# Kernel tuning notes

Measured on AMD Instinct MI355X. Metric: run time of the kernel, lower is better.

## Reference

```python
import jax, jax.numpy as jnp
import numpy as np

B, S, D = 32, 8192, 128
SPARSITY = 0.5
CLUSTER = 4
HID = 256
MEM = 128
NCLS = 10
MASK_KEY = jax.random.key(1234)


def setup_inputs() -> dict:
    key = jax.random.key(0)
    ks = jax.random.split(key, 8)
    cin = CLUSTER * D  # 512
    return {
        "x": jax.random.normal(ks[0], (B, S, D), dtype=jnp.float32),
        "memory": jax.random.normal(ks[1], (B, MEM), dtype=jnp.float32),
        "W_fc": jax.random.normal(ks[2], (HID, cin), dtype=jnp.float32) / np.sqrt(cin),
        "b_fc": jax.random.normal(ks[3], (HID,), dtype=jnp.float32) * 0.01,
        "W_mem": jax.random.normal(ks[4], (MEM, HID), dtype=jnp.float32) / np.sqrt(HID),
        "b_mem": jax.random.normal(ks[5], (MEM,), dtype=jnp.float32) * 0.01,
        "W_out": jax.random.normal(ks[6], (NCLS, MEM), dtype=jnp.float32) / np.sqrt(MEM),
        "b_out": jax.random.normal(ks[7], (NCLS,), dtype=jnp.float32) * 0.01,
    }


def reference(x, memory, W_fc, b_fc, W_mem, b_mem, W_out, b_out):
    # --- SparseInformationExtraction: top-k tokens by L2 norm ---
    k = int(SPARSITY * S)  # 4096
    token_norms = jnp.linalg.norm(x, axis=-1)          # (B, S)
    _, topk_idx = jax.lax.top_k(token_norms, k)        # (B, k), sorted desc like torch.topk
    sparse_x = jnp.take_along_axis(x, topk_idx[:, :, None], axis=1)  # (B, k, D)

    # --- HierarchicalClustering: group CLUSTER tokens ---
    num_clusters = k // CLUSTER                        # 1024
    clustered = sparse_x.reshape(B, num_clusters, CLUSTER * D)  # (B, 1024, 512)

    # --- DynamicMaskingActivation: linear + bernoulli mask + relu ---
    h = jnp.einsum('bnc,hc->bnh', clustered, W_fc) + b_fc       # (B, 1024, HID)
    mask = jax.random.bernoulli(MASK_KEY, p=SPARSITY, shape=h.shape).astype(h.dtype)
    h = jax.nn.relu(h * mask)

    # --- SparseMemory: mean-pool + linear + residual relu ---
    x_compressed = jnp.mean(h, axis=1)                           # (B, HID)
    updated_memory = jax.nn.relu(x_compressed @ W_mem.T + b_mem + memory)  # (B, MEM)

    # --- output head ---
    output = updated_memory @ W_out.T + b_out                    # (B, NCLS)
    return (output, updated_memory)
```

## Files before the change

### kernel.cpp

```cpp
#include <hip/hip_runtime.h>
#include <stdint.h>

#define NB 32
#define NS 8192
#define ND 128
#define KTOP 4096
#define NCLUST 1024
#define CIN 512
#define HIDN 256
#define NMEM 128
#define NCLS 10
#define HALFCNT 4194304u

typedef unsigned long long ull;
typedef __attribute__((ext_vector_type(8))) short bf16x8;
typedef __attribute__((ext_vector_type(4))) float f32x4;

__device__ __forceinline__ unsigned int rotl32(unsigned int v, int r) {
  return (v << r) | (v >> (32 - r));
}

__device__ __forceinline__ void threefry_block(unsigned int& x0, unsigned int& x1) {
  const unsigned int k0 = 0u;
  const unsigned int k1 = 1234u;
  const unsigned int k2 = 0x1BD11BDAu ^ 0u ^ 1234u;
  x0 += k0; x1 += k1;
#define TF_R(r) { x0 += x1; x1 = rotl32(x1, (r)); x1 ^= x0; }
  TF_R(13) TF_R(15) TF_R(26) TF_R(6)   x0 += k1; x1 += k2 + 1u;
  TF_R(17) TF_R(29) TF_R(16) TF_R(24)  x0 += k2; x1 += k0 + 2u;
  TF_R(13) TF_R(15) TF_R(26) TF_R(6)   x0 += k0; x1 += k1 + 3u;
  TF_R(17) TF_R(29) TF_R(16) TF_R(24)  x0 += k1; x1 += k2 + 4u;
  TF_R(13) TF_R(15) TF_R(26) TF_R(6)   x0 += k2; x1 += k0 + 5u;
#undef TF_R
}

__device__ __forceinline__ unsigned int f2bf(float f) {
  unsigned int u = __float_as_uint(f);
  return (u + 0x7fffu + ((u >> 16) & 1u)) >> 16;
}
__device__ __forceinline__ unsigned int pack2bf(float lo, float hi) {
  return f2bf(lo) | (f2bf(hi) << 16);
}

__device__ __forceinline__ void gload_lds16(const void* g, void* l) {
  __builtin_amdgcn_global_load_lds(
      (const __attribute__((address_space(1))) unsigned int*)g,
      (__attribute__((address_space(3))) unsigned int*)l, 16, 0, 0);
}

__device__ __forceinline__ ull shfl_xor_u64(ull x, int m) {
  unsigned int lo = (unsigned int)x, hi = (unsigned int)(x >> 32);
  lo = (unsigned int)__shfl_xor((int)lo, m);
  hi = (unsigned int)__shfl_xor((int)hi, m);
  return ((ull)hi << 32) | lo;
}

#define NORM_BLOCKS 32768
#define WPREP_BLOCKS 64
#define MASK_BLOCKS 16384
__global__ __launch_bounds__(256) void norms_kernel(
    const float* __restrict__ x, ull* __restrict__ keys,
    float* __restrict__ xc, const float* __restrict__ Wfc,
    unsigned short* __restrict__ Wbf, ull* __restrict__ maskw) {
  const int blk = blockIdx.x;
  if (blk >= NORM_BLOCKS + WPREP_BLOCKS) {
    const int blkm = blk - (NORM_BLOCKS + WPREP_BLOCKS);
    const int wv = threadIdx.x >> 6, lane = threadIdx.x & 63;
    const unsigned int W = (unsigned int)(blkm * 4 + wv);
    unsigned int a = W * 64u + (unsigned int)lane;
    unsigned int b2 = a + HALFCNT;
    threefry_block(a, b2);
    const ull m0 = __ballot((a & 0x80000000u) == 0u);
    const ull m1 = __ballot((b2 & 0x80000000u) == 0u);
    if (lane == 0) {
      maskw[W] = m0;
      maskw[W + 65536u] = m1;
    }
    return;
  }
  if (blk >= NORM_BLOCKS) {
    const int t = (blk - NORM_BLOCKS) * 256 + threadIdx.x;
    const float4* s = (const float4*)(Wfc + (size_t)t * 8);
    const float4 a = s[0], b = s[1];
    uint4 o;
    o.x = pack2bf(a.x, a.y); o.y = pack2bf(a.z, a.w);
    o.z = pack2bf(b.x, b.y); o.w = pack2bf(b.z, b.w);
    *(uint4*)(Wbf + (size_t)t * 8) = o;
    return;
  }
  const int t = blk * 256 + threadIdx.x;
  if (t < NB * HIDN) xc[t] = 0.0f;
  const int token = t >> 5;
  const int l = t & 31;
  const float4 v = ((const float4*)(x + (size_t)token * ND))[l];
  float ss = v.x * v.x + v.y * v.y + v.z * v.z + v.w * v.w;
#pragma unroll
  for (int off = 16; off >= 1; off >>= 1) ss += __shfl_xor(ss, off);
  if (l == 0) {
    const float nrm = sqrtf(ss);
    const unsigned int ub = ~__float_as_uint(nrm);
    keys[token] = ((ull)ub << 32) | (unsigned int)(token & (NS - 1));
  }
}

#define CMPEX(J, K, HF)                                                 \
  {                                                                     \
    _Pragma("unroll") for (int r = 0; r < 8; ++r) {                     \
      if ((r & (J)) == 0) {                                             \
        const int i0 = (tid << 3) + r;                                  \
        const bool up2 = (((i0 & (K)) == 0) != (HF));                   \
        const ull lo = v[r], hi = v[r | (J)];                           \
        const ull mn = lo < hi ? lo : hi;                               \
        const ull mx = lo < hi ? hi : lo;                               \
        v[r] = up2 ? mn : mx;                                           \
        v[r | (J)] = up2 ? mx : mn;                                     \
      }                                                                 \
    }                                                                   \
  }

__global__ __launch_bounds__(512) void sortA_kernel(ull* __restrict__ keys) {
  __shared__ ull slds[8 * 512];
  const int b = blockIdx.x >> 1;
  const int half = blockIdx.x & 1;
  const bool hf = (half != 0);
  const int tid = threadIdx.x;
  ull v[8];
  ull* base = keys + (size_t)b * NS + half * 4096;
#pragma unroll
  for (int r = 0; r < 8; ++r) v[r] = base[tid * 8 + r];

  for (int k = 2; k <= 4096; k <<= 1) {
    for (int j = k >> 1; j >= 512; j >>= 1) {
      __syncthreads();
#pragma unroll
      for (int r = 0; r < 8; ++r) slds[r * 512 + tid] = v[r];
      __syncthreads();
      const int ptid = tid ^ (j >> 3);
      const bool up2 = ((((tid << 3) & k) == 0) != hf);
      const bool lower = (((tid << 3) & j) == 0);
      const bool keepmin = (up2 == lower);
#pragma unroll
      for (int r = 0; r < 8; ++r) {
        const ull p = slds[r * 512 + ptid];
        const ull mn = v[r] < p ? v[r] : p;
        const ull mx = v[r] < p ? p : v[r];
        v[r] = keepmin ? mn : mx;
      }
    }
    {
      const int jstart = (k >> 1) < 256 ? (k >> 1) : 256;
      for (int j = jstart; j >= 8; j >>= 1) {
        const int lanemask = j >> 3;
        const bool up2 = ((((tid << 3) & k) == 0) != hf);
        const bool lower = (((tid << 3) & j) == 0);
        const bool keepmin = (up2 == lower);
#pragma unroll
        for (int r = 0; r < 8; ++r) {
          const ull p = shfl_xor_u64(v[r], lanemask);
          const ull mn = v[r] < p ? v[r] : p;
          const ull mx = v[r] < p ? p : v[r];
          v[r] = keepmin ? mn : mx;
        }
      }
    }
    if (k >= 8)      { CMPEX(4, k, hf) CMPEX(2, k, hf) CMPEX(1, k, hf) }
    else if (k == 4) { CMPEX(2, k, hf) CMPEX(1, k, hf) }
    else             { CMPEX(1, k, hf) }
  }

#pragma unroll
  for (int r = 0; r < 8; ++r) base[tid * 8 + r] = v[r];
}

__global__ __launch_bounds__(512) void sortB_kernel(
    const ull* __restrict__ keys, unsigned int* __restrict__ topk) {
  __shared__ ull slds[8 * 512];
  const int b = blockIdx.x;
  const int tid = threadIdx.x;
  ull v[8];
  const ull* base = keys + (size_t)b * NS;
#pragma unroll
  for (int r = 0; r < 8; ++r) v[r] = base[tid * 8 + r];
#pragma unroll
  for (int r = 0; r < 8; ++r) {
    const ull u = base[4096 + tid * 8 + r];
    v[r] = v[r] < u ? v[r] : u;
  }
  for (int j = 2048; j >= 512; j >>= 1) {
    __syncthreads();
#pragma unroll
    for (int r = 0; r < 8; ++r) slds[r * 512 + tid] = v[r];
    __syncthreads();
    const int ptid = tid ^ (j >> 3);
    const bool keepmin = (((tid << 3) & j) == 0);
#pragma unroll
    for (int r = 0; r < 8; ++r) {
      const ull p = slds[r * 512 + ptid];
      const ull mn = v[r] < p ? v[r] : p;
      const ull mx = v[r] < p ? p : v[r];
      v[r] = keepmin ? mn : mx;
    }
  }
  for (int j = 256; j >= 8; j >>= 1) {
    const int lanemask = j >> 3;
    const bool keepmin = (((tid << 3) & j) == 0);
#pragma unroll
    for (int r = 0; r < 8; ++r) {
      const ull p = shfl_xor_u64(v[r], lanemask);
      const ull mn = v[r] < p ? v[r] : p;
      const ull mx = v[r] < p ? p : v[r];
      v[r] = keepmin ? mn : mx;
    }
  }
  CMPEX(4, 8192, false) CMPEX(2, 8192, false) CMPEX(1, 8192, false)
#pragma unroll
  for (int r = 0; r < 8; ++r)
    topk[b * KTOP + tid * 8 + r] = (unsigned int)v[r];
}

__global__ __launch_bounds__(256, 4) void gemm_kernel(
    const float* __restrict__ x, const unsigned short* __restrict__ Wbf,
    const float* __restrict__ bfc, const unsigned int* __restrict__ topk,
    const ull* __restrict__ maskw, float* __restrict__ xc) {
  __shared__ __align__(16) unsigned short Al[32 * 64];
  __shared__ __align__(16) unsigned short Bl[256 * 64];
  __shared__ int tokL[128];

  const int bid = blockIdx.x;
  const int bb = bid >> 5;
  const int m0c = (bid & 31) * 32;
  const int t = threadIdx.x;
  const int w = t >> 6, l = t & 63;
  const int lrow = l & 15, lk = l >> 4;

  if (t < 128)
    tokL[t] = (int)topk[bb * KTOP + (m0c + (t >> 2)) * 4 + (t & 3)];
  __syncthreads();

  const int arow = t >> 3, kq = t & 7;
  float4 ar[16];
  {
    const float* xb = x + (size_t)bb * NS * ND;
#pragma unroll
    for (int kt = 0; kt < 8; ++kt) {
      const int cs = kt * 8 + kq;
      const int token = tokL[arow * 4 + (cs >> 4)];
      const float* asrc = xb + (size_t)token * ND + (cs & 15) * 8;
      ar[kt * 2]     = ((const float4*)asrc)[0];
      ar[kt * 2 + 1] = ((const float4*)asrc)[1];
    }
  }

  f32x4 acc[2][4];
#pragma unroll
  for (int m = 0; m < 2; ++m)
#pragma unroll
    for (int n = 0; n < 4; ++n) acc[m][n] = (f32x4)0.f;

  const int brow_in8 = l >> 3;
  const int bkb_src = ((l & 7) * 16) ^ (brow_in8 << 4);

  for (int kt = 0; kt < 8; ++kt) {
    {
      const float4 a0 = ar[kt * 2], a1 = ar[kt * 2 + 1];
      uint4 p0;
      p0.x = pack2bf(a0.x, a0.y); p0.y = pack2bf(a0.z, a0.w);
      p0.z = pack2bf(a1.x, a1.y); p0.w = pack2bf(a1.z, a1.w);
      const int swz = (arow & 7) << 4;
      *(uint4*)((char*)Al + arow * 128 + ((kq * 16) ^ swz)) = p0;
    }
    {
#pragma unroll
      for (int q = 0; q < 8; ++q) {
        const int grp = w * 8 + q;
        const int row = grp * 8 + brow_in8;
        const char* g = (const char*)Wbf + (size_t)row * 1024 + kt * 128 +
                        bkb_src;
        gload_lds16(g, (char*)Bl + grp * 1024);
      }
    }
    __syncthreads();

    const int swz = (lrow & 7) << 4;
#pragma unroll
    for (int kk = 0; kk < 2; ++kk) {
      const int koff = (kk * 64 + lk * 16) ^ swz;
      bf16x8 af[2], bfr[4];
#pragma unroll
      for (int m = 0; m < 2; ++m)
        af[m] = *(const bf16x8*)((const char*)Al +
                                 (m * 16 + lrow) * 128 + koff);
#pragma unroll
      for (int n = 0; n < 4; ++n)
        bfr[n] = *(const bf16x8*)((const char*)Bl +
                                  (w * 64 + n * 16 + lrow) * 128 + koff);
#pragma unroll
      for (int m = 0; m < 2; ++m)
#pragma unroll
        for (int n = 0; n < 4; ++n)
          acc[m][n] = __builtin_amdgcn_mfma_f32_16x16x32_bf16(
              af[m], bfr[n], acc[m][n], 0, 0, 0);
    }
    __syncthreads();
  }

  float bias_n[4];
#pragma unroll
  for (int n = 0; n < 4; ++n) bias_n[n] = bfc[w * 64 + n * 16 + lrow];

  ull mw[2][4];
#pragma unroll
  for (int m = 0; m < 2; ++m)
#pragma unroll
    for (int reg = 0; reg < 4; ++reg) {
      const int row = m0c + m * 16 + lk * 4 + reg;
      mw[m][reg] = maskw[(size_t)(bb * NCLUST + row) * 4 + w];
    }

  float csum[4] = {0.f, 0.f, 0.f, 0.f};
#pragma unroll
  for (int n = 0; n < 4; ++n) {
    const int bit = n * 16 + lrow;
#pragma unroll
    for (int m = 0; m < 2; ++m) {
#pragma unroll
      for (int reg = 0; reg < 4; ++reg) {
        const bool keep = ((mw[m][reg] >> bit) & 1ull) != 0ull;
        float vv = acc[m][n][reg] + bias_n[n];
        vv = keep ? fmaxf(vv, 0.0f) : 0.0f;
        csum[n] += vv;
      }
    }
  }
#pragma unroll
  for (int n = 0; n < 4; ++n) {
    csum[n] += __shfl_xor(csum[n], 16);
    csum[n] += __shfl_xor(csum[n], 32);
  }
  if (l < 16) {
#pragma unroll
    for (int n = 0; n < 4; ++n)
      atomicAdd(&xc[bb * HIDN + w * 64 + n * 16 + l], csum[n]);
  }
}

__global__ __launch_bounds__(128) void tail_kernel(
    const float* __restrict__ xc, const float* __restrict__ memory,
    const float* __restrict__ Wmem, const float* __restrict__ bmem,
    const float* __restrict__ Wout, const float* __restrict__ bout,
    float* __restrict__ out) {
  __shared__ __align__(16) float xl[HIDN];
  __shared__ float ul[NMEM];
  const int b = blockIdx.x, t = threadIdx.x;
  xl[t]       = xc[b * HIDN + t] * (1.0f / NCLUST);
  xl[t + 128] = xc[b * HIDN + t + 128] * (1.0f / NCLUST);
  __syncthreads();
  float a = 0.0f;
  const float4* wr2 = (const float4*)(Wmem + (size_t)t * HIDN);
#pragma unroll 4
  for (int q = 0; q < HIDN / 4; ++q) {
    const float4 wv = wr2[q];
    const float4 xv = *(const float4*)&xl[q * 4];
    a = fmaf(wv.x, xv.x, a); a = fmaf(wv.y, xv.y, a);
    a = fmaf(wv.z, xv.z, a); a = fmaf(wv.w, xv.w, a);
  }
  a += bmem[t] + memory[b * NMEM + t];
  a = fmaxf(a, 0.0f);
  ul[t] = a;
  out[NB * NCLS + b * NMEM + t] = a;
  __syncthreads();
  if (t < NCLS) {
    float o = 0.0f;
#pragma unroll 4
    for (int m = 0; m < NMEM; ++m) o = fmaf(ul[m], Wout[t * NMEM + m], o);
    out[b * NCLS + t] = o + bout[t];
  }
}

extern "C" void kernel_launch(void* const* d_in, const int* in_sizes, int n_in,
                              void* d_out, int out_size, void* d_ws, size_t ws_size,
                              hipStream_t stream) {
  (void)in_sizes; (void)n_in; (void)out_size; (void)ws_size;
  const float* x    = (const float*)d_in[0];
  const float* mem  = (const float*)d_in[1];
  const float* Wfc  = (const float*)d_in[2];
  const float* bfc  = (const float*)d_in[3];
  const float* Wmem = (const float*)d_in[4];
  const float* bmem = (const float*)d_in[5];
  const float* Wout = (const float*)d_in[6];
  const float* bout = (const float*)d_in[7];
  float* out = (float*)d_out;

  char* ws = (char*)d_ws;
  size_t off = 0;
  ull* keys = (ull*)(ws + off);          off += (size_t)NB * NS * 8;
  unsigned int* topk = (unsigned int*)(ws + off); off += (size_t)NB * KTOP * 4;
  float* xc = (float*)(ws + off);        off += (size_t)NB * HIDN * 4;
  unsigned short* Wbf = (unsigned short*)(ws + off); off += (size_t)HIDN * CIN * 2;
  ull* maskw = (ull*)(ws + off);

  norms_kernel<<<dim3(NORM_BLOCKS + WPREP_BLOCKS + MASK_BLOCKS), 256, 0,
                 stream>>>(x, keys, xc, Wfc, Wbf, maskw);
  sortA_kernel<<<dim3(NB * 2), 512, 0, stream>>>(keys);
  sortB_kernel<<<dim3(NB), 512, 0, stream>>>(keys, topk);
  gemm_kernel<<<dim3(1024), 256, 0, stream>>>(x, Wbf, bfc, topk, maskw, xc);
  tail_kernel<<<dim3(NB), 128, 0, stream>>>(xc, mem, Wmem, bmem, Wout, bout, out);
}
```

Measured before the change: 276.8 us.

## Split token gather into separate bf16 packing kernel before GEMM

Adds a gather kernel that reads the top-k tokens from x, converts them to bf16, and writes a contiguous clustered A matrix to workspace. The GEMM then loads A tiles with direct global-to-LDS copies instead of holding 16 float4 registers per thread and packing them itself, which cuts register pressure and scattered loads inside the GEMM. In exchange it adds a kernel launch and an extra round trip of about 8 MB of bf16 data through global memory.

```diff
diff --git a/kernel.cpp b/kernel.cpp
--- a/kernel.cpp
+++ b/kernel.cpp
@@ -218,13 +218,30 @@
     topk[b * KTOP + tid * 8 + r] = (unsigned int)v[r];
 }
 
+__global__ __launch_bounds__(256) void gather_kernel(
+    const float* __restrict__ x, const unsigned int* __restrict__ topk,
+    unsigned short* __restrict__ Ap) {
+  const int blk = blockIdx.x;
+  const int bb = blk >> 8;
+  const int c = (blk & 255) * 4 + (threadIdx.x >> 6);
+  const int lane = threadIdx.x & 63;
+  const int token = (int)topk[bb * KTOP + c * 4 + (lane >> 4)];
+  const float* src = x + ((size_t)bb * NS + token) * ND + (lane & 15) * 8;
+  const float4 a0 = ((const float4*)src)[0];
+  const float4 a1 = ((const float4*)src)[1];
+  uint4 p;
+  p.x = pack2bf(a0.x, a0.y); p.y = pack2bf(a0.z, a0.w);
+  p.z = pack2bf(a1.x, a1.y); p.w = pack2bf(a1.z, a1.w);
+  *(uint4*)(Ap + (size_t)(bb * NCLUST + c) * 512 + lane * 8) = p;
+}
+
 __global__ __launch_bounds__(256, 4) void gemm_kernel(
-    const float* __restrict__ x, const unsigned short* __restrict__ Wbf,
-    const float* __restrict__ bfc, const unsigned int* __restrict__ topk,
-    const ull* __restrict__ maskw, float* __restrict__ xc) {
+    const unsigned short* __restrict__ Ap,
+    const unsigned short* __restrict__ Wbf,
+    const float* __restrict__ bfc, const ull* __restrict__ maskw,
+    float* __restrict__ xc) {
   __shared__ __align__(16) unsigned short Al[32 * 64];
   __shared__ __align__(16) unsigned short Bl[256 * 64];
-  __shared__ int tokL[128];
 
   const int bid = blockIdx.x;
   const int bb = bid >> 5;
@@ -233,51 +250,28 @@
   const int w = t >> 6, l = t & 63;
   const int lrow = l & 15, lk = l >> 4;
 
-  if (t < 128)
-    tokL[t] = (int)topk[bb * KTOP + (m0c + (t >> 2)) * 4 + (t & 3)];
-  __syncthreads();
-
-  const int arow = t >> 3, kq = t & 7;
-  float4 ar[16];
-  {
-    const float* xb = x + (size_t)bb * NS * ND;
-#pragma unroll
-    for (int kt = 0; kt < 8; ++kt) {
-      const int cs = kt * 8 + kq;
-      const int token = tokL[arow * 4 + (cs >> 4)];
-      const float* asrc = xb + (size_t)token * ND + (cs & 15) * 8;
-      ar[kt * 2]     = ((const float4*)asrc)[0];
-      ar[kt * 2 + 1] = ((const float4*)asrc)[1];
-    }
-  }
-
-  f32x4 acc[2][4];
-#pragma unroll
-  for (int m = 0; m < 2; ++m)
-#pragma unroll
-    for (int n = 0; n < 4; ++n) acc[m][n] = (f32x4)0.f;
-
+  const int arow = t >> 3, aseg = t & 7;
+  const char* abase = (const char*)Ap +
+                      (size_t)(bb * NCLUST + m0c + arow) * 1024 +
+                      ((aseg * 16) ^ ((arow & 7) << 4));
   const int brow_in8 = l >> 3;
   const int bkb_src = ((l & 7) * 16) ^ (brow_in8 << 4);
 
+  f32x4 acc[2][4];
+#pragma unroll
+  for (int m = 0; m < 2; ++m)
+#pragma unroll
+    for (int n = 0; n < 4; ++n) acc[m][n] = (f32x4)0.f;
+
   for (int kt = 0; kt < 8; ++kt) {
-    {
-      const float4 a0 = ar[kt * 2], a1 = ar[kt * 2 + 1];
-      uint4 p0;
-      p0.x = pack2bf(a0.x, a0.y); p0.y = pack2bf(a0.z, a0.w);
-      p0.z = pack2bf(a1.x, a1.y); p0.w = pack2bf(a1.z, a1.w);
-      const int swz = (arow & 7) << 4;
-      *(uint4*)((char*)Al + arow * 128 + ((kq * 16) ^ swz)) = p0;
-    }
-    {
-#pragma unroll
-      for (int q = 0; q < 8; ++q) {
-        const int grp = w * 8 + q;
-        const int row = grp * 8 + brow_in8;
-        const char* g = (const char*)Wbf + (size_t)row * 1024 + kt * 128 +
-                        bkb_src;
-        gload_lds16(g, (char*)Bl + grp * 1024);
-      }
+    gload_lds16(abase + kt * 128, (char*)Al + t * 16);
+#pragma unroll
+    for (int q = 0; q < 8; ++q) {
+      const int grp = w * 8 + q;
+      const int row = grp * 8 + brow_in8;
+      const char* g = (const char*)Wbf + (size_t)row * 1024 + kt * 128 +
+                      bkb_src;
+      gload_lds16(g, (char*)Bl + grp * 1024);
     }
     __syncthreads();
 
@@ -397,12 +391,14 @@
   unsigned int* topk = (unsigned int*)(ws + off); off += (size_t)NB * KTOP * 4;
   float* xc = (float*)(ws + off);        off += (size_t)NB * HIDN * 4;
   unsigned short* Wbf = (unsigned short*)(ws + off); off += (size_t)HIDN * CIN * 2;
-  ull* maskw = (ull*)(ws + off);
+  ull* maskw = (ull*)(ws + off);         off += (size_t)131072 * 8;
+  unsigned short* Ap = (unsigned short*)(ws + off);
 
   norms_kernel<<<dim3(NORM_BLOCKS + WPREP_BLOCKS + MASK_BLOCKS), 256, 0,
                  stream>>>(x, keys, xc, Wfc, Wbf, maskw);
   sortA_kernel<<<dim3(NB * 2), 512, 0, stream>>>(keys);
   sortB_kernel<<<dim3(NB), 512, 0, stream>>>(keys, topk);
-  gemm_kernel<<<dim3(1024), 256, 0, stream>>>(x, Wbf, bfc, topk, maskw, xc);
+  gather_kernel<<<dim3(NB * 256), 256, 0, stream>>>(x, topk, Ap);
+  gemm_kernel<<<dim3(1024), 256, 0, stream>>>(Ap, Wbf, bfc, maskw, xc);
   tail_kernel<<<dim3(NB), 128, 0, stream>>>(xc, mem, Wmem, bmem, Wout, bout, out);
 }
```

Result: no change. 279.6 us (+1.0%).
